# Performance work log

Measured on AMD Instinct MI355X. Metric: run time of the kernel, lower is better.

Reference implementation:

```python
import jax, jax.numpy as jnp
import numpy as np

N_NODES = 50000


def gcn_conv(x, edge_index, W, b, n_nodes):
    # Linear transform first (as in PyG GCNConv), then normalized aggregation
    xw = x @ W  # [N, out]
    src, dst = edge_index[0], edge_index[1]
    loops = jnp.arange(n_nodes, dtype=src.dtype)
    s = jnp.concatenate([src, loops])  # add self-loops
    d = jnp.concatenate([dst, loops])
    deg = jax.ops.segment_sum(jnp.ones_like(s, dtype=xw.dtype), d, num_segments=n_nodes)
    dinv = jnp.where(deg > 0, jax.lax.rsqrt(deg), 0.0)
    norm = dinv[s] * dinv[d]  # [E+N]
    msg = xw[s] * norm[:, None]  # gather + scale
    out = jax.ops.segment_sum(msg, d, num_segments=n_nodes)  # scatter-add
    return out + b


def setup_inputs() -> dict:
    key = jax.random.key(0)
    k1, k2, k3, k4 = jax.random.split(key, 4)
    in_dim, hidden = 128, 128
    n_edges = 625000
    x = jax.random.normal(k1, (N_NODES, in_dim), dtype=jnp.float32)
    edge_index = jax.random.randint(k2, (2, n_edges), 0, N_NODES, dtype=jnp.int64)
    # glorot-ish scale
    W1 = jax.random.normal(k3, (in_dim, hidden), dtype=jnp.float32) * (1.0 / np.sqrt(in_dim))
    b1 = jnp.zeros((hidden,), dtype=jnp.float32)
    W2 = jax.random.normal(k4, (hidden, hidden), dtype=jnp.float32) * (1.0 / np.sqrt(hidden))
    b2 = jnp.zeros((hidden,), dtype=jnp.float32)
    return {"x": x, "edge_index": edge_index, "W1": W1, "b1": b1, "W2": W2, "b2": b2}


def reference(x, edge_index, W1, b1, W2, b2):
    n = x.shape[0]
    h = gcn_conv(x, edge_index, W1, b1, n)
    h = jax.nn.relu(h)
    # dropout(p=0.3) is identity in eval mode
    h = gcn_conv(h, edge_index, W2, b2, n)
    return jax.nn.relu(h)
```

## Files before the change

kernel.cpp:

```cpp
#include <hip/hip_runtime.h>
#include <hip/hip_bf16.h>

#define NNODES 50000
#define BKT 64
#define LP 136

typedef short bf16x8 __attribute__((ext_vector_type(8)));
typedef float f32x4 __attribute__((ext_vector_type(4)));

__device__ __forceinline__ unsigned short f2bf_rn(float f) {
    unsigned int u = __float_as_uint(f);
    return (unsigned short)((u + 0x7fffu + ((u >> 16) & 1u)) >> 16);
}
__device__ __forceinline__ float bf_lo(unsigned int u) { return __uint_as_float(u << 16); }
__device__ __forceinline__ float bf_hi(unsigned int u) { return __uint_as_float(u & 0xffff0000u); }


__global__ __launch_bounds__(256) void k_wt(const float* __restrict__ W1,
                                            const float* __restrict__ W2,
                                            unsigned short* __restrict__ WT1,
                                            unsigned short* __restrict__ WT2,
                                            int* __restrict__ cnt, int N) {
    __shared__ float tile[128 * 129];
    int b = blockIdx.x, t = threadIdx.x;
    if (b < 2) {
        const float* W = b ? W2 : W1;
        unsigned short* WT = b ? WT2 : WT1;
        for (int idx = t; idx < 128 * 128; idx += 256)
            tile[(idx >> 7) * 129 + (idx & 127)] = W[idx];
        __syncthreads();
        for (int idx = t; idx < 128 * 128; idx += 256) {
            int c = idx >> 7, k = idx & 127;
            WT[c * 128 + k] = f2bf_rn(tile[k * 129 + c]);
        }
    } else {
        int i = (b - 2) * 256 + t;
        if (i < N) cnt[i] = 0;
    }
}


__device__ __forceinline__ void gather_accum(const unsigned int* __restrict__ xwb,
                                             const int* __restrict__ cnt,
                                             const int* __restrict__ bp,
                                             int degc, int lane,
                                             float& ax, float& ay) {
    float px = 0.f, py = 0.f;
    int j = 0;
    for (; j + 8 <= degc; j += 8) {
        int4 q0 = *(const int4*)&bp[j];
        int4 q1 = *(const int4*)&bp[j + 4];
        unsigned int u0 = xwb[(size_t)q0.x * 64 + lane];
        unsigned int u1 = xwb[(size_t)q0.y * 64 + lane];
        unsigned int u2 = xwb[(size_t)q0.z * 64 + lane];
        unsigned int u3 = xwb[(size_t)q0.w * 64 + lane];
        unsigned int u4 = xwb[(size_t)q1.x * 64 + lane];
        unsigned int u5 = xwb[(size_t)q1.y * 64 + lane];
        unsigned int u6 = xwb[(size_t)q1.z * 64 + lane];
        unsigned int u7 = xwb[(size_t)q1.w * 64 + lane];
        float w0 = rsqrtf((float)cnt[q0.x] + 1.0f), w1 = rsqrtf((float)cnt[q0.y] + 1.0f);
        float w2 = rsqrtf((float)cnt[q0.z] + 1.0f), w3 = rsqrtf((float)cnt[q0.w] + 1.0f);
        float w4 = rsqrtf((float)cnt[q1.x] + 1.0f), w5 = rsqrtf((float)cnt[q1.y] + 1.0f);
        float w6 = rsqrtf((float)cnt[q1.z] + 1.0f), w7 = rsqrtf((float)cnt[q1.w] + 1.0f);
        ax = fmaf(bf_lo(u0), w0, ax);  ay = fmaf(bf_hi(u0), w0, ay);
        px = fmaf(bf_lo(u1), w1, px);  py = fmaf(bf_hi(u1), w1, py);
        ax = fmaf(bf_lo(u2), w2, ax);  ay = fmaf(bf_hi(u2), w2, ay);
        px = fmaf(bf_lo(u3), w3, px);  py = fmaf(bf_hi(u3), w3, py);
        ax = fmaf(bf_lo(u4), w4, ax);  ay = fmaf(bf_hi(u4), w4, ay);
        px = fmaf(bf_lo(u5), w5, px);  py = fmaf(bf_hi(u5), w5, py);
        ax = fmaf(bf_lo(u6), w6, ax);  ay = fmaf(bf_hi(u6), w6, ay);
        px = fmaf(bf_lo(u7), w7, px);  py = fmaf(bf_hi(u7), w7, py);
    }
    if (j + 4 <= degc) {
        int4 q = *(const int4*)&bp[j];
        unsigned int u0 = xwb[(size_t)q.x * 64 + lane];
        unsigned int u1 = xwb[(size_t)q.y * 64 + lane];
        unsigned int u2 = xwb[(size_t)q.z * 64 + lane];
        unsigned int u3 = xwb[(size_t)q.w * 64 + lane];
        float w0 = rsqrtf((float)cnt[q.x] + 1.0f), w1 = rsqrtf((float)cnt[q.y] + 1.0f);
        float w2 = rsqrtf((float)cnt[q.z] + 1.0f), w3 = rsqrtf((float)cnt[q.w] + 1.0f);
        ax = fmaf(bf_lo(u0), w0, ax);  ay = fmaf(bf_hi(u0), w0, ay);
        px = fmaf(bf_lo(u1), w1, px);  py = fmaf(bf_hi(u1), w1, py);
        ax = fmaf(bf_lo(u2), w2, ax);  ay = fmaf(bf_hi(u2), w2, ay);
        px = fmaf(bf_lo(u3), w3, px);  py = fmaf(bf_hi(u3), w3, py);
        j += 4;
    }
    for (; j < degc; ++j) {
        int s = bp[j];
        float wv = rsqrtf((float)cnt[s] + 1.0f);
        unsigned int u = xwb[(size_t)s * 64 + lane];
        ax = fmaf(bf_lo(u), wv, ax);
        ay = fmaf(bf_hi(u), wv, ay);
    }
    ax += px;
    ay += py;
}


__global__ __launch_bounds__(256) void k_gemmbucket(const float* __restrict__ X,
                                                    const unsigned short* __restrict__ WT,
                                                    unsigned short* __restrict__ Yb, int n,
                                                    const int* __restrict__ src,
                                                    const int* __restrict__ dst,
                                                    int* __restrict__ cnt,
                                                    int* __restrict__ bkt, int E, int EB) {
    __shared__ unsigned short Wl[128 * LP];
    int t = threadIdx.x;
    if ((int)blockIdx.x < EB) {
        int e = blockIdx.x * 256 + t;
        if (e < E) {
            int s = src[e], d = dst[e];
            int pos = atomicAdd(&cnt[d], 1);
            if (pos < BKT) bkt[(size_t)d * BKT + pos] = s;
        }
        return;
    }
    int gb = blockIdx.x - EB;
    int lane = t & 63, w = t >> 6;
    int m = lane & 15, quad = lane >> 4;
    int base = gb * 64 + w * 16;
    int row = min(base + m, n - 1);

    bf16x8 a[4];
#pragma unroll
    for (int kt = 0; kt < 4; ++kt) {
        const float* pa = &X[(size_t)row * 128 + kt * 32 + quad * 8];
        float4 v0 = *(const float4*)pa;
        float4 v1 = *(const float4*)(pa + 4);
        a[kt][0] = (short)f2bf_rn(v0.x); a[kt][1] = (short)f2bf_rn(v0.y);
        a[kt][2] = (short)f2bf_rn(v0.z); a[kt][3] = (short)f2bf_rn(v0.w);
        a[kt][4] = (short)f2bf_rn(v1.x); a[kt][5] = (short)f2bf_rn(v1.y);
        a[kt][6] = (short)f2bf_rn(v1.z); a[kt][7] = (short)f2bf_rn(v1.w);
    }
    for (int idx = t; idx < 128 * 16; idx += 256) {
        int r = idx >> 4, c8 = (idx & 15) << 3;
        *(uint4*)&Wl[r * LP + c8] = *(const uint4*)&WT[r * 128 + c8];
    }
    __syncthreads();

    f32x4 acc[8];
#pragma unroll
    for (int i = 0; i < 8; ++i) acc[i] = f32x4{0.f, 0.f, 0.f, 0.f};
#pragma unroll
    for (int kt = 0; kt < 4; ++kt) {
        int ko = kt * 32 + quad * 8;
#pragma unroll
        for (int ct = 0; ct < 8; ++ct) {
            bf16x8 b = *(const bf16x8*)&Wl[(ct * 16 + m) * LP + ko];
            acc[ct] = __builtin_amdgcn_mfma_f32_16x16x32_bf16(a[kt], b, acc[ct], 0, 0, 0);
        }
    }
    __syncthreads();

    unsigned short* ep = &Wl[w * 16 * LP];
#pragma unroll
    for (int ct = 0; ct < 8; ++ct)
#pragma unroll
        for (int r = 0; r < 4; ++r)
            ep[(quad * 4 + r) * LP + ct * 16 + m] = f2bf_rn(acc[ct][r]);
    __syncthreads();
    int rr = lane & 15, cc = lane >> 4;
    int orow = base + rr;
    if (orow < n) {
#pragma unroll
        for (int i2 = 0; i2 < 4; ++i2)
            ((uint4*)&Yb[(size_t)orow * 128])[cc * 4 + i2] =
                *(const uint4*)&ep[rr * LP + (cc * 4 + i2) * 8];
    }
}


__global__ __launch_bounds__(1024, 2) void k_aggemm(const unsigned int* __restrict__ xw1,
                                                    const int* __restrict__ cnt,
                                                    const int* __restrict__ bkt,
                                                    const float* __restrict__ bias,
                                                    const unsigned short* __restrict__ WT2,
                                                    unsigned short* __restrict__ xw2, int n) {
    __shared__ unsigned short Wl[128 * LP];
    __shared__ unsigned short At[16 * LP];
    int t = threadIdx.x, lane = t & 63, w = t >> 6;
    int base = blockIdx.x * 16;

    for (int idx = t; idx < 128 * 16; idx += 1024) {
        int r = idx >> 4, c8 = (idx & 15) << 3;
        *(uint4*)&Wl[r * LP + c8] = *(const uint4*)&WT2[r * 128 + c8];
    }

    int i = min(base + w, n - 1);
    int deg = cnt[i];
    int degc = min(deg, BKT);
    float di = rsqrtf((float)deg + 1.0f);
    unsigned int v0 = xw1[(size_t)i * 64 + lane];
    float ax = di * bf_lo(v0), ay = di * bf_hi(v0);
    gather_accum(xw1, cnt, &bkt[(size_t)i * BKT], degc, lane, ax, ay);
    float bx = bias[lane * 2], by = bias[lane * 2 + 1];
    ax = fmaxf(fmaf(di, ax, bx), 0.0f);
    ay = fmaxf(fmaf(di, ay, by), 0.0f);
    ((unsigned int*)&At[w * LP])[lane] = (unsigned)f2bf_rn(ax) | ((unsigned)f2bf_rn(ay) << 16);
    __syncthreads();

    int m = lane & 15, quad = lane >> 4;
    f32x4 acc = f32x4{0.f, 0.f, 0.f, 0.f};
    if (w < 8) {
        bf16x8 a[4];
#pragma unroll
        for (int kt = 0; kt < 4; ++kt)
            a[kt] = *(const bf16x8*)&At[m * LP + kt * 32 + quad * 8];
#pragma unroll
        for (int kt = 0; kt < 4; ++kt) {
            bf16x8 b = *(const bf16x8*)&Wl[(w * 16 + m) * LP + kt * 32 + quad * 8];
            acc = __builtin_amdgcn_mfma_f32_16x16x32_bf16(a[kt], b, acc, 0, 0, 0);
        }
    }
    __syncthreads();
    if (w < 8) {
#pragma unroll
        for (int r = 0; r < 4; ++r)
            At[(quad * 4 + r) * LP + w * 16 + m] = f2bf_rn(acc[r]);
    }
    __syncthreads();
    if (t < 256) {
        int row = t >> 4, q = t & 15;
        int orow = base + row;
        if (orow < n)
            *(uint4*)&xw2[(size_t)orow * 128 + q * 8] = *(const uint4*)&At[row * LP + q * 8];
    }
}


__global__ __launch_bounds__(256) void k_agg(const unsigned int* __restrict__ xwb,
                                             const int* __restrict__ cnt,
                                             const int* __restrict__ bkt,
                                             const float* __restrict__ bias,
                                             float* __restrict__ out, int n) {
    int lane = threadIdx.x & 63;
    int i = (blockIdx.x * 256 + threadIdx.x) >> 6;
    if (i >= n) return;
    int deg = cnt[i];
    int degc = min(deg, BKT);
    float di = rsqrtf((float)deg + 1.0f);
    unsigned int v0 = xwb[(size_t)i * 64 + lane];
    float ax = di * bf_lo(v0), ay = di * bf_hi(v0);
    gather_accum(xwb, cnt, &bkt[(size_t)i * BKT], degc, lane, ax, ay);
    float bx = bias[lane * 2], by = bias[lane * 2 + 1];
    ax = fmaxf(fmaf(di, ax, bx), 0.0f);
    ay = fmaxf(fmaf(di, ay, by), 0.0f);
    ((float2*)out)[(size_t)i * 64 + lane] = make_float2(ax, ay);
}


extern "C" void kernel_launch(void* const* d_in, const int* in_sizes, int n_in,
                              void* d_out, int out_size, void* d_ws, size_t ws_size,
                              hipStream_t stream) {
    const float* x  = (const float*)d_in[0];
    const int*   ei = (const int*)d_in[1];
    const float* W1 = (const float*)d_in[2];
    const float* b1 = (const float*)d_in[3];
    const float* W2 = (const float*)d_in[4];
    const float* b2 = (const float*)d_in[5];
    float* out = (float*)d_out;

    const int N = NNODES;
    const int E = in_sizes[1] / 2;
    const int* src = ei;
    const int* dst = ei + E;

    char* p = (char*)d_ws;
    size_t off = 0;
    auto take = [&](size_t bytes) -> void* {
        void* r = p + off;
        off = (off + bytes + 255) & ~(size_t)255;
        return r;
    };
    int* cnt = (int*)take((size_t)N * 4);
    int* bkt = (int*)take((size_t)N * BKT * 4);
    unsigned short* w1t = (unsigned short*)take(128 * 128 * 2);
    unsigned short* w2t = (unsigned short*)take(128 * 128 * 2);
    unsigned short* xw1 = (unsigned short*)take((size_t)N * 128 * 2);
    unsigned short* xw2 = (unsigned short*)take((size_t)N * 128 * 2);

    const int NB = (N + 255) / 256;
    const int EB = (E + 255) / 256;
    const int GB = (N + 63) / 64;

    k_wt<<<2 + NB, 256, 0, stream>>>(W1, W2, w1t, w2t, cnt, N);
    k_gemmbucket<<<EB + GB, 256, 0, stream>>>(x, w1t, xw1, N, src, dst, cnt, bkt, E, EB);
    k_aggemm<<<(N + 15) / 16, 1024, 0, stream>>>((const unsigned int*)xw1, cnt, bkt,
                                                 b1, w2t, xw2, N);
    k_agg<<<(N * 64 + 255) / 256, 256, 0, stream>>>((const unsigned int*)xw2, cnt, bkt,
                                                    b2, out, N);
}
```

Before: 205.7 us.

## Prescale GEMM outputs by source degree norm and shrink bucket indices to u16

Folds the per-source rsqrt(deg) factor into the GEMM epilogues, so the gather loops become plain adds with no per-neighbour count lookups. Bucket indices are stored as 16-bit values, which halves index traffic. The bucketing moves into a prep kernel that handles four edges per thread, and the count reset becomes a memset. The cost is that the layer-1 GEMM now waits for bucketing to finish instead of running alongside it, and the 16-bit indices only work while the node count stays below 65536.

```diff
diff --git a/kernel.cpp b/kernel.cpp
--- a/kernel.cpp
+++ b/kernel.cpp
@@ -16,110 +16,107 @@
 __device__ __forceinline__ float bf_hi(unsigned int u) { return __uint_as_float(u & 0xffff0000u); }
 
 
-__global__ __launch_bounds__(256) void k_wt(const float* __restrict__ W1,
-                                            const float* __restrict__ W2,
-                                            unsigned short* __restrict__ WT1,
-                                            unsigned short* __restrict__ WT2,
-                                            int* __restrict__ cnt, int N) {
-    __shared__ float tile[128 * 129];
+__global__ __launch_bounds__(256) void k_prep(const float* __restrict__ W1,
+                                              const float* __restrict__ W2,
+                                              unsigned short* __restrict__ WT1,
+                                              unsigned short* __restrict__ WT2,
+                                              const int* __restrict__ src,
+                                              const int* __restrict__ dst,
+                                              int* __restrict__ cnt,
+                                              unsigned short* __restrict__ bkt,
+                                              int E, int S) {
     int b = blockIdx.x, t = threadIdx.x;
     if (b < 2) {
         const float* W = b ? W2 : W1;
         unsigned short* WT = b ? WT2 : WT1;
-        for (int idx = t; idx < 128 * 128; idx += 256)
-            tile[(idx >> 7) * 129 + (idx & 127)] = W[idx];
-        __syncthreads();
         for (int idx = t; idx < 128 * 128; idx += 256) {
-            int c = idx >> 7, k = idx & 127;
-            WT[c * 128 + k] = f2bf_rn(tile[k * 129 + c]);
+            int k = idx >> 7, c = idx & 127;
+            WT[c * 128 + k] = f2bf_rn(W[idx]);
         }
-    } else {
-        int i = (b - 2) * 256 + t;
-        if (i < N) cnt[i] = 0;
-    }
-}
-
-
-__device__ __forceinline__ void gather_accum(const unsigned int* __restrict__ xwb,
-                                             const int* __restrict__ cnt,
-                                             const int* __restrict__ bp,
-                                             int degc, int lane,
-                                             float& ax, float& ay) {
+        return;
+    }
+    int tid = (b - 2) * 256 + t;
+    int e0 = tid, e1 = tid + S, e2 = tid + 2 * S, e3 = tid + 3 * S;
+    int s0 = 0, s1 = 0, s2 = 0, s3 = 0, d0 = 0, d1 = 0, d2 = 0, d3 = 0;
+    if (e0 < E) { s0 = src[e0]; d0 = dst[e0]; }
+    if (e1 < E) { s1 = src[e1]; d1 = dst[e1]; }
+    if (e2 < E) { s2 = src[e2]; d2 = dst[e2]; }
+    if (e3 < E) { s3 = src[e3]; d3 = dst[e3]; }
+    if (e0 < E) { int p = atomicAdd(&cnt[d0], 1); if (p < BKT) bkt[(size_t)d0 * BKT + p] = (unsigned short)s0; }
+    if (e1 < E) { int p = atomicAdd(&cnt[d1], 1); if (p < BKT) bkt[(size_t)d1 * BKT + p] = (unsigned short)s1; }
+    if (e2 < E) { int p = atomicAdd(&cnt[d2], 1); if (p < BKT) bkt[(size_t)d2 * BKT + p] = (unsigned short)s2; }
+    if (e3 < E) { int p = atomicAdd(&cnt[d3], 1); if (p < BKT) bkt[(size_t)d3 * BKT + p] = (unsigned short)s3; }
+}
+
+
+__device__ __forceinline__ void gather_add(const unsigned int* __restrict__ xwb,
+                                           const unsigned short* __restrict__ bp,
+                                           int degc, int lane,
+                                           float& ax, float& ay) {
     float px = 0.f, py = 0.f;
     int j = 0;
     for (; j + 8 <= degc; j += 8) {
-        int4 q0 = *(const int4*)&bp[j];
-        int4 q1 = *(const int4*)&bp[j + 4];
-        unsigned int u0 = xwb[(size_t)q0.x * 64 + lane];
-        unsigned int u1 = xwb[(size_t)q0.y * 64 + lane];
-        unsigned int u2 = xwb[(size_t)q0.z * 64 + lane];
-        unsigned int u3 = xwb[(size_t)q0.w * 64 + lane];
-        unsigned int u4 = xwb[(size_t)q1.x * 64 + lane];
-        unsigned int u5 = xwb[(size_t)q1.y * 64 + lane];
-        unsigned int u6 = xwb[(size_t)q1.z * 64 + lane];
-        unsigned int u7 = xwb[(size_t)q1.w * 64 + lane];
-        float w0 = rsqrtf((float)cnt[q0.x] + 1.0f), w1 = rsqrtf((float)cnt[q0.y] + 1.0f);
-        float w2 = rsqrtf((float)cnt[q0.z] + 1.0f), w3 = rsqrtf((float)cnt[q0.w] + 1.0f);
-        float w4 = rsqrtf((float)cnt[q1.x] + 1.0f), w5 = rsqrtf((float)cnt[q1.y] + 1.0f);
-        float w6 = rsqrtf((float)cnt[q1.z] + 1.0f), w7 = rsqrtf((float)cnt[q1.w] + 1.0f);
-        ax = fmaf(bf_lo(u0), w0, ax);  ay = fmaf(bf_hi(u0), w0, ay);
-        px = fmaf(bf_lo(u1), w1, px);  py = fmaf(bf_hi(u1), w1, py);
-        ax = fmaf(bf_lo(u2), w2, ax);  ay = fmaf(bf_hi(u2), w2, ay);
-        px = fmaf(bf_lo(u3), w3, px);  py = fmaf(bf_hi(u3), w3, py);
-        ax = fmaf(bf_lo(u4), w4, ax);  ay = fmaf(bf_hi(u4), w4, ay);
-        px = fmaf(bf_lo(u5), w5, px);  py = fmaf(bf_hi(u5), w5, py);
-        ax = fmaf(bf_lo(u6), w6, ax);  ay = fmaf(bf_hi(u6), w6, ay);
-        px = fmaf(bf_lo(u7), w7, px);  py = fmaf(bf_hi(u7), w7, py);
+        uint4 q = *(const uint4*)&bp[j];
+        int s0 = q.x & 0xffff, s1 = q.x >> 16;
+        int s2 = q.y & 0xffff, s3 = q.y >> 16;
+        int s4 = q.z & 0xffff, s5 = q.z >> 16;
+        int s6 = q.w & 0xffff, s7 = q.w >> 16;
+        unsigned int u0 = xwb[(size_t)s0 * 64 + lane];
+        unsigned int u1 = xwb[(size_t)s1 * 64 + lane];
+        unsigned int u2 = xwb[(size_t)s2 * 64 + lane];
+        unsigned int u3 = xwb[(size_t)s3 * 64 + lane];
+        unsigned int u4 = xwb[(size_t)s4 * 64 + lane];
+        unsigned int u5 = xwb[(size_t)s5 * 64 + lane];
+        unsigned int u6 = xwb[(size_t)s6 * 64 + lane];
+        unsigned int u7 = xwb[(size_t)s7 * 64 + lane];
+        ax += bf_lo(u0);  ay += bf_hi(u0);
+        px += bf_lo(u1);  py += bf_hi(u1);
+        ax += bf_lo(u2);  ay += bf_hi(u2);
+        px += bf_lo(u3);  py += bf_hi(u3);
+        ax += bf_lo(u4);  ay += bf_hi(u4);
+        px += bf_lo(u5);  py += bf_hi(u5);
+        ax += bf_lo(u6);  ay += bf_hi(u6);
+        px += bf_lo(u7);  py += bf_hi(u7);
     }
     if (j + 4 <= degc) {
-        int4 q = *(const int4*)&bp[j];
-        unsigned int u0 = xwb[(size_t)q.x * 64 + lane];
-        unsigned int u1 = xwb[(size_t)q.y * 64 + lane];
-        unsigned int u2 = xwb[(size_t)q.z * 64 + lane];
-        unsigned int u3 = xwb[(size_t)q.w * 64 + lane];
-        float w0 = rsqrtf((float)cnt[q.x] + 1.0f), w1 = rsqrtf((float)cnt[q.y] + 1.0f);
-        float w2 = rsqrtf((float)cnt[q.z] + 1.0f), w3 = rsqrtf((float)cnt[q.w] + 1.0f);
-        ax = fmaf(bf_lo(u0), w0, ax);  ay = fmaf(bf_hi(u0), w0, ay);
-        px = fmaf(bf_lo(u1), w1, px);  py = fmaf(bf_hi(u1), w1, py);
-        ax = fmaf(bf_lo(u2), w2, ax);  ay = fmaf(bf_hi(u2), w2, ay);
-        px = fmaf(bf_lo(u3), w3, px);  py = fmaf(bf_hi(u3), w3, py);
+        uint2 q = *(const uint2*)&bp[j];
+        int s0 = q.x & 0xffff, s1 = q.x >> 16;
+        int s2 = q.y & 0xffff, s3 = q.y >> 16;
+        unsigned int u0 = xwb[(size_t)s0 * 64 + lane];
+        unsigned int u1 = xwb[(size_t)s1 * 64 + lane];
+        unsigned int u2 = xwb[(size_t)s2 * 64 + lane];
+        unsigned int u3 = xwb[(size_t)s3 * 64 + lane];
+        ax += bf_lo(u0);  ay += bf_hi(u0);
+        px += bf_lo(u1);  py += bf_hi(u1);
+        ax += bf_lo(u2);  ay += bf_hi(u2);
+        px += bf_lo(u3);  py += bf_hi(u3);
         j += 4;
     }
     for (; j < degc; ++j) {
         int s = bp[j];
-        float wv = rsqrtf((float)cnt[s] + 1.0f);
         unsigned int u = xwb[(size_t)s * 64 + lane];
-        ax = fmaf(bf_lo(u), wv, ax);
-        ay = fmaf(bf_hi(u), wv, ay);
+        ax += bf_lo(u);
+        ay += bf_hi(u);
     }
     ax += px;
     ay += py;
 }
 
 
-__global__ __launch_bounds__(256) void k_gemmbucket(const float* __restrict__ X,
-                                                    const unsigned short* __restrict__ WT,
-                                                    unsigned short* __restrict__ Yb, int n,
-                                                    const int* __restrict__ src,
-                                                    const int* __restrict__ dst,
-                                                    int* __restrict__ cnt,
-                                                    int* __restrict__ bkt, int E, int EB) {
+__global__ __launch_bounds__(256) void k_gemm1(const float* __restrict__ X,
+                                               const unsigned short* __restrict__ WT,
+                                               const int* __restrict__ cnt,
+                                               unsigned short* __restrict__ Yb, int n) {
     __shared__ unsigned short Wl[128 * LP];
-    int t = threadIdx.x;
-    if ((int)blockIdx.x < EB) {
-        int e = blockIdx.x * 256 + t;
-        if (e < E) {
-            int s = src[e], d = dst[e];
-            int pos = atomicAdd(&cnt[d], 1);
-            if (pos < BKT) bkt[(size_t)d * BKT + pos] = s;
-        }
-        return;
-    }
-    int gb = blockIdx.x - EB;
-    int lane = t & 63, w = t >> 6;
+    int t = threadIdx.x, lane = t & 63, w = t >> 6;
     int m = lane & 15, quad = lane >> 4;
-    int base = gb * 64 + w * 16;
+    int base = blockIdx.x * 64 + w * 16;
     int row = min(base + m, n - 1);
+
+    float di_r[4];
+#pragma unroll
+    for (int r = 0; r < 4; ++r)
+        di_r[r] = rsqrtf((float)cnt[min(base + quad * 4 + r, n - 1)] + 1.0f);
 
     bf16x8 a[4];
 #pragma unroll
@@ -146,8 +143,8 @@
         int ko = kt * 32 + quad * 8;
 #pragma unroll
         for (int ct = 0; ct < 8; ++ct) {
-            bf16x8 b = *(const bf16x8*)&Wl[(ct * 16 + m) * LP + ko];
-            acc[ct] = __builtin_amdgcn_mfma_f32_16x16x32_bf16(a[kt], b, acc[ct], 0, 0, 0);
+            bf16x8 bb = *(const bf16x8*)&Wl[(ct * 16 + m) * LP + ko];
+            acc[ct] = __builtin_amdgcn_mfma_f32_16x16x32_bf16(a[kt], bb, acc[ct], 0, 0, 0);
         }
     }
     __syncthreads();
@@ -157,7 +154,7 @@
     for (int ct = 0; ct < 8; ++ct)
 #pragma unroll
         for (int r = 0; r < 4; ++r)
-            ep[(quad * 4 + r) * LP + ct * 16 + m] = f2bf_rn(acc[ct][r]);
+            ep[(quad * 4 + r) * LP + ct * 16 + m] = f2bf_rn(acc[ct][r] * di_r[r]);
     __syncthreads();
     int rr = lane & 15, cc = lane >> 4;
     int orow = base + rr;
@@ -172,14 +169,20 @@
 
 __global__ __launch_bounds__(1024, 2) void k_aggemm(const unsigned int* __restrict__ xw1,
                                                     const int* __restrict__ cnt,
-                                                    const int* __restrict__ bkt,
+                                                    const unsigned short* __restrict__ bkt,
                                                     const float* __restrict__ bias,
                                                     const unsigned short* __restrict__ WT2,
                                                     unsigned short* __restrict__ xw2, int n) {
     __shared__ unsigned short Wl[128 * LP];
     __shared__ unsigned short At[16 * LP];
     int t = threadIdx.x, lane = t & 63, w = t >> 6;
+    int m = lane & 15, quad = lane >> 4;
     int base = blockIdx.x * 16;
+
+    float di_e[4];
+#pragma unroll
+    for (int r = 0; r < 4; ++r)
+        di_e[r] = rsqrtf((float)cnt[min(base + quad * 4 + r, n - 1)] + 1.0f);
 
     for (int idx = t; idx < 128 * 16; idx += 1024) {
         int r = idx >> 4, c8 = (idx & 15) << 3;
@@ -191,15 +194,14 @@
     int degc = min(deg, BKT);
     float di = rsqrtf((float)deg + 1.0f);
     unsigned int v0 = xw1[(size_t)i * 64 + lane];
-    float ax = di * bf_lo(v0), ay = di * bf_hi(v0);
-    gather_accum(xw1, cnt, &bkt[(size_t)i * BKT], degc, lane, ax, ay);
+    float ax = bf_lo(v0), ay = bf_hi(v0);
+    gather_add(xw1, &bkt[(size_t)i * BKT], degc, lane, ax, ay);
     float bx = bias[lane * 2], by = bias[lane * 2 + 1];
     ax = fmaxf(fmaf(di, ax, bx), 0.0f);
     ay = fmaxf(fmaf(di, ay, by), 0.0f);
     ((unsigned int*)&At[w * LP])[lane] = (unsigned)f2bf_rn(ax) | ((unsigned)f2bf_rn(ay) << 16);
     __syncthreads();
 
-    int m = lane & 15, quad = lane >> 4;
     f32x4 acc = f32x4{0.f, 0.f, 0.f, 0.f};
     if (w < 8) {
         bf16x8 a[4];
@@ -208,15 +210,15 @@
             a[kt] = *(const bf16x8*)&At[m * LP + kt * 32 + quad * 8];
 #pragma unroll
         for (int kt = 0; kt < 4; ++kt) {
-            bf16x8 b = *(const bf16x8*)&Wl[(w * 16 + m) * LP + kt * 32 + quad * 8];
-            acc = __builtin_amdgcn_mfma_f32_16x16x32_bf16(a[kt], b, acc, 0, 0, 0);
+            bf16x8 bb = *(const bf16x8*)&Wl[(w * 16 + m) * LP + kt * 32 + quad * 8];
+            acc = __builtin_amdgcn_mfma_f32_16x16x32_bf16(a[kt], bb, acc, 0, 0, 0);
         }
     }
     __syncthreads();
     if (w < 8) {
 #pragma unroll
         for (int r = 0; r < 4; ++r)
-            At[(quad * 4 + r) * LP + w * 16 + m] = f2bf_rn(acc[r]);
+            At[(quad * 4 + r) * LP + w * 16 + m] = f2bf_rn(acc[r] * di_e[r]);
     }
     __syncthreads();
     if (t < 256) {
@@ -230,7 +232,7 @@
 
 __global__ __launch_bounds__(256) void k_agg(const unsigned int* __restrict__ xwb,
                                              const int* __restrict__ cnt,
-                                             const int* __restrict__ bkt,
+                                             const unsigned short* __restrict__ bkt,
                                              const float* __restrict__ bias,
                                              float* __restrict__ out, int n) {
     int lane = threadIdx.x & 63;
@@ -240,8 +242,8 @@
     int degc = min(deg, BKT);
     float di = rsqrtf((float)deg + 1.0f);
     unsigned int v0 = xwb[(size_t)i * 64 + lane];
-    float ax = di * bf_lo(v0), ay = di * bf_hi(v0);
-    gather_accum(xwb, cnt, &bkt[(size_t)i * BKT], degc, lane, ax, ay);
+    float ax = bf_lo(v0), ay = bf_hi(v0);
+    gather_add(xwb, &bkt[(size_t)i * BKT], degc, lane, ax, ay);
     float bx = bias[lane * 2], by = bias[lane * 2 + 1];
     ax = fmaxf(fmaf(di, ax, bx), 0.0f);
     ay = fmaxf(fmaf(di, ay, by), 0.0f);
@@ -273,18 +275,19 @@
         return r;
     };
     int* cnt = (int*)take((size_t)N * 4);
-    int* bkt = (int*)take((size_t)N * BKT * 4);
+    unsigned short* bkt = (unsigned short*)take((size_t)N * BKT * 2);
     unsigned short* w1t = (unsigned short*)take(128 * 128 * 2);
     unsigned short* w2t = (unsigned short*)take(128 * 128 * 2);
     unsigned short* xw1 = (unsigned short*)take((size_t)N * 128 * 2);
     unsigned short* xw2 = (unsigned short*)take((size_t)N * 128 * 2);
 
-    const int NB = (N + 255) / 256;
-    const int EB = (E + 255) / 256;
+    const int BB = (E + 4 * 256 - 1) / (4 * 256);
+    const int S  = BB * 256;
     const int GB = (N + 63) / 64;
 
-    k_wt<<<2 + NB, 256, 0, stream>>>(W1, W2, w1t, w2t, cnt, N);
-    k_gemmbucket<<<EB + GB, 256, 0, stream>>>(x, w1t, xw1, N, src, dst, cnt, bkt, E, EB);
+    hipMemsetAsync(cnt, 0, (size_t)N * 4, stream);
+    k_prep<<<2 + BB, 256, 0, stream>>>(W1, W2, w1t, w2t, src, dst, cnt, bkt, E, S);
+    k_gemm1<<<GB, 256, 0, stream>>>(x, w1t, cnt, xw1, N);
     k_aggemm<<<(N + 15) / 16, 1024, 0, stream>>>((const unsigned int*)xw1, cnt, bkt,
                                                  b1, w2t, xw2, N);
     k_agg<<<(N * 64 + 255) / 256, 256, 0, stream>>>((const unsigned int*)xw2, cnt, bkt,
```

New measurement: 211.9 us. 3.0% more time.

## Pack neighbor indices to 16-bit, gather with 16-byte loads, prescale second-layer features

Applied to the files above, without the earlier changes.

Bucket indices are stored as unsigned short instead of int, which halves bucket memory traffic. The aggregation kernels now map four nodes per wavefront, with 16 lanes each loading 16-byte vectors instead of 4-byte words. The layer-2 GEMM output is pre-multiplied by the source node's dinv, so the final aggregation skips the per-neighbor count lookups and rsqrt. The fused aggregation-GEMM kernel also processes 64 rows per block instead of 16. Risks: 16-bit indices only hold node ids below 65536, and loop predication now runs by wavefront via __any.

```diff
diff --git a/kernel.cpp b/kernel.cpp
--- a/kernel.cpp
+++ b/kernel.cpp
@@ -14,6 +14,13 @@
 }
 __device__ __forceinline__ float bf_lo(unsigned int u) { return __uint_as_float(u << 16); }
 __device__ __forceinline__ float bf_hi(unsigned int u) { return __uint_as_float(u & 0xffff0000u); }
+
+__device__ __forceinline__ void acc8(float* a, uint4 u, float wv) {
+    a[0] = fmaf(bf_lo(u.x), wv, a[0]);  a[1] = fmaf(bf_hi(u.x), wv, a[1]);
+    a[2] = fmaf(bf_lo(u.y), wv, a[2]);  a[3] = fmaf(bf_hi(u.y), wv, a[3]);
+    a[4] = fmaf(bf_lo(u.z), wv, a[4]);  a[5] = fmaf(bf_hi(u.z), wv, a[5]);
+    a[6] = fmaf(bf_lo(u.w), wv, a[6]);  a[7] = fmaf(bf_hi(u.w), wv, a[7]);
+}
 
 
 __global__ __launch_bounds__(256) void k_wt(const float* __restrict__ W1,
@@ -40,70 +47,14 @@
 }
 
 
-__device__ __forceinline__ void gather_accum(const unsigned int* __restrict__ xwb,
-                                             const int* __restrict__ cnt,
-                                             const int* __restrict__ bp,
-                                             int degc, int lane,
-                                             float& ax, float& ay) {
-    float px = 0.f, py = 0.f;
-    int j = 0;
-    for (; j + 8 <= degc; j += 8) {
-        int4 q0 = *(const int4*)&bp[j];
-        int4 q1 = *(const int4*)&bp[j + 4];
-        unsigned int u0 = xwb[(size_t)q0.x * 64 + lane];
-        unsigned int u1 = xwb[(size_t)q0.y * 64 + lane];
-        unsigned int u2 = xwb[(size_t)q0.z * 64 + lane];
-        unsigned int u3 = xwb[(size_t)q0.w * 64 + lane];
-        unsigned int u4 = xwb[(size_t)q1.x * 64 + lane];
-        unsigned int u5 = xwb[(size_t)q1.y * 64 + lane];
-        unsigned int u6 = xwb[(size_t)q1.z * 64 + lane];
-        unsigned int u7 = xwb[(size_t)q1.w * 64 + lane];
-        float w0 = rsqrtf((float)cnt[q0.x] + 1.0f), w1 = rsqrtf((float)cnt[q0.y] + 1.0f);
-        float w2 = rsqrtf((float)cnt[q0.z] + 1.0f), w3 = rsqrtf((float)cnt[q0.w] + 1.0f);
-        float w4 = rsqrtf((float)cnt[q1.x] + 1.0f), w5 = rsqrtf((float)cnt[q1.y] + 1.0f);
-        float w6 = rsqrtf((float)cnt[q1.z] + 1.0f), w7 = rsqrtf((float)cnt[q1.w] + 1.0f);
-        ax = fmaf(bf_lo(u0), w0, ax);  ay = fmaf(bf_hi(u0), w0, ay);
-        px = fmaf(bf_lo(u1), w1, px);  py = fmaf(bf_hi(u1), w1, py);
-        ax = fmaf(bf_lo(u2), w2, ax);  ay = fmaf(bf_hi(u2), w2, ay);
-        px = fmaf(bf_lo(u3), w3, px);  py = fmaf(bf_hi(u3), w3, py);
-        ax = fmaf(bf_lo(u4), w4, ax);  ay = fmaf(bf_hi(u4), w4, ay);
-        px = fmaf(bf_lo(u5), w5, px);  py = fmaf(bf_hi(u5), w5, py);
-        ax = fmaf(bf_lo(u6), w6, ax);  ay = fmaf(bf_hi(u6), w6, ay);
-        px = fmaf(bf_lo(u7), w7, px);  py = fmaf(bf_hi(u7), w7, py);
-    }
-    if (j + 4 <= degc) {
-        int4 q = *(const int4*)&bp[j];
-        unsigned int u0 = xwb[(size_t)q.x * 64 + lane];
-        unsigned int u1 = xwb[(size_t)q.y * 64 + lane];
-        unsigned int u2 = xwb[(size_t)q.z * 64 + lane];
-        unsigned int u3 = xwb[(size_t)q.w * 64 + lane];
-        float w0 = rsqrtf((float)cnt[q.x] + 1.0f), w1 = rsqrtf((float)cnt[q.y] + 1.0f);
-        float w2 = rsqrtf((float)cnt[q.z] + 1.0f), w3 = rsqrtf((float)cnt[q.w] + 1.0f);
-        ax = fmaf(bf_lo(u0), w0, ax);  ay = fmaf(bf_hi(u0), w0, ay);
-        px = fmaf(bf_lo(u1), w1, px);  py = fmaf(bf_hi(u1), w1, py);
-        ax = fmaf(bf_lo(u2), w2, ax);  ay = fmaf(bf_hi(u2), w2, ay);
-        px = fmaf(bf_lo(u3), w3, px);  py = fmaf(bf_hi(u3), w3, py);
-        j += 4;
-    }
-    for (; j < degc; ++j) {
-        int s = bp[j];
-        float wv = rsqrtf((float)cnt[s] + 1.0f);
-        unsigned int u = xwb[(size_t)s * 64 + lane];
-        ax = fmaf(bf_lo(u), wv, ax);
-        ay = fmaf(bf_hi(u), wv, ay);
-    }
-    ax += px;
-    ay += py;
-}
-
-
 __global__ __launch_bounds__(256) void k_gemmbucket(const float* __restrict__ X,
                                                     const unsigned short* __restrict__ WT,
                                                     unsigned short* __restrict__ Yb, int n,
                                                     const int* __restrict__ src,
                                                     const int* __restrict__ dst,
                                                     int* __restrict__ cnt,
-                                                    int* __restrict__ bkt, int E, int EB) {
+                                                    unsigned short* __restrict__ bkt,
+                                                    int E, int EB) {
     __shared__ unsigned short Wl[128 * LP];
     int t = threadIdx.x;
     if ((int)blockIdx.x < EB) {
@@ -111,7 +62,7 @@
         if (e < E) {
             int s = src[e], d = dst[e];
             int pos = atomicAdd(&cnt[d], 1);
-            if (pos < BKT) bkt[(size_t)d * BKT + pos] = s;
+            if (pos < BKT) bkt[(size_t)d * BKT + pos] = (unsigned short)s;
         }
         return;
     }
@@ -146,8 +97,8 @@
         int ko = kt * 32 + quad * 8;
 #pragma unroll
         for (int ct = 0; ct < 8; ++ct) {
-            bf16x8 b = *(const bf16x8*)&Wl[(ct * 16 + m) * LP + ko];
-            acc[ct] = __builtin_amdgcn_mfma_f32_16x16x32_bf16(a[kt], b, acc[ct], 0, 0, 0);
+            bf16x8 bb = *(const bf16x8*)&Wl[(ct * 16 + m) * LP + ko];
+            acc[ct] = __builtin_amdgcn_mfma_f32_16x16x32_bf16(a[kt], bb, acc[ct], 0, 0, 0);
         }
     }
     __syncthreads();
@@ -170,82 +121,159 @@
 }
 
 
-__global__ __launch_bounds__(1024, 2) void k_aggemm(const unsigned int* __restrict__ xw1,
+__global__ __launch_bounds__(1024, 2) void k_aggemm(const unsigned int* __restrict__ xw1u,
                                                     const int* __restrict__ cnt,
-                                                    const int* __restrict__ bkt,
+                                                    const unsigned short* __restrict__ bkt,
                                                     const float* __restrict__ bias,
                                                     const unsigned short* __restrict__ WT2,
                                                     unsigned short* __restrict__ xw2, int n) {
     __shared__ unsigned short Wl[128 * LP];
-    __shared__ unsigned short At[16 * LP];
+    __shared__ unsigned short At[64 * LP];
     int t = threadIdx.x, lane = t & 63, w = t >> 6;
-    int base = blockIdx.x * 16;
+    int base = blockIdx.x * 64;
 
     for (int idx = t; idx < 128 * 16; idx += 1024) {
         int r = idx >> 4, c8 = (idx & 15) << 3;
         *(uint4*)&Wl[r * LP + c8] = *(const uint4*)&WT2[r * 128 + c8];
     }
 
-    int i = min(base + w, n - 1);
-    int deg = cnt[i];
-    int degc = min(deg, BKT);
+    int g = lane >> 4, li = lane & 15;
+    int node = min(base + w * 4 + g, n - 1);
+    int deg = cnt[node], degc = min(deg, BKT);
     float di = rsqrtf((float)deg + 1.0f);
-    unsigned int v0 = xw1[(size_t)i * 64 + lane];
-    float ax = di * bf_lo(v0), ay = di * bf_hi(v0);
-    gather_accum(xw1, cnt, &bkt[(size_t)i * BKT], degc, lane, ax, ay);
-    float bx = bias[lane * 2], by = bias[lane * 2 + 1];
-    ax = fmaxf(fmaf(di, ax, bx), 0.0f);
-    ay = fmaxf(fmaf(di, ay, by), 0.0f);
-    ((unsigned int*)&At[w * LP])[lane] = (unsigned)f2bf_rn(ax) | ((unsigned)f2bf_rn(ay) << 16);
-    __syncthreads();
+    uint4 v = *(const uint4*)&xw1u[(size_t)node * 64 + li * 4];
+    float a[8];
+    a[0] = di * bf_lo(v.x);  a[1] = di * bf_hi(v.x);
+    a[2] = di * bf_lo(v.y);  a[3] = di * bf_hi(v.y);
+    a[4] = di * bf_lo(v.z);  a[5] = di * bf_hi(v.z);
+    a[6] = di * bf_lo(v.w);  a[7] = di * bf_hi(v.w);
+    const unsigned short* bp = &bkt[(size_t)node * BKT];
+    for (int j = 0; __any(j < degc); j += 8) {
+        if (j < degc) {
+            uint4 q = *(const uint4*)&bp[j];
+            int s0 = q.x & 0xffff, s1 = q.x >> 16, s2 = q.y & 0xffff, s3 = q.y >> 16;
+            int s4 = q.z & 0xffff, s5 = q.z >> 16, s6 = q.w & 0xffff, s7 = q.w >> 16;
+            uint4 u0 = *(const uint4*)&xw1u[(size_t)s0 * 64 + li * 4];
+            uint4 u1 = *(const uint4*)&xw1u[(size_t)s1 * 64 + li * 4];
+            uint4 u2 = *(const uint4*)&xw1u[(size_t)s2 * 64 + li * 4];
+            uint4 u3 = *(const uint4*)&xw1u[(size_t)s3 * 64 + li * 4];
+            uint4 u4 = *(const uint4*)&xw1u[(size_t)s4 * 64 + li * 4];
+            uint4 u5 = *(const uint4*)&xw1u[(size_t)s5 * 64 + li * 4];
+            uint4 u6 = *(const uint4*)&xw1u[(size_t)s6 * 64 + li * 4];
+            uint4 u7 = *(const uint4*)&xw1u[(size_t)s7 * 64 + li * 4];
+            float w0 = (j + 0 < degc) ? rsqrtf((float)cnt[s0] + 1.0f) : 0.0f;
+            float w1 = (j + 1 < degc) ? rsqrtf((float)cnt[s1] + 1.0f) : 0.0f;
+            float w2 = (j + 2 < degc) ? rsqrtf((float)cnt[s2] + 1.0f) : 0.0f;
+            float w3 = (j + 3 < degc) ? rsqrtf((float)cnt[s3] + 1.0f) : 0.0f;
+            float w4 = (j + 4 < degc) ? rsqrtf((float)cnt[s4] + 1.0f) : 0.0f;
+            float w5 = (j + 5 < degc) ? rsqrtf((float)cnt[s5] + 1.0f) : 0.0f;
+            float w6 = (j + 6 < degc) ? rsqrtf((float)cnt[s6] + 1.0f) : 0.0f;
+            float w7 = (j + 7 < degc) ? rsqrtf((float)cnt[s7] + 1.0f) : 0.0f;
+            acc8(a, u0, w0); acc8(a, u1, w1); acc8(a, u2, w2); acc8(a, u3, w3);
+            acc8(a, u4, w4); acc8(a, u5, w5); acc8(a, u6, w6); acc8(a, u7, w7);
+        }
+    }
+    float4 b0 = ((const float4*)bias)[li * 2];
+    float4 b1v = ((const float4*)bias)[li * 2 + 1];
+    float h0 = fmaxf(fmaf(di, a[0], b0.x), 0.f), h1 = fmaxf(fmaf(di, a[1], b0.y), 0.f);
+    float h2 = fmaxf(fmaf(di, a[2], b0.z), 0.f), h3 = fmaxf(fmaf(di, a[3], b0.w), 0.f);
+    float h4 = fmaxf(fmaf(di, a[4], b1v.x), 0.f), h5 = fmaxf(fmaf(di, a[5], b1v.y), 0.f);
+    float h6 = fmaxf(fmaf(di, a[6], b1v.z), 0.f), h7 = fmaxf(fmaf(di, a[7], b1v.w), 0.f);
+    uint4 hp;
+    hp.x = (unsigned)f2bf_rn(h0) | ((unsigned)f2bf_rn(h1) << 16);
+    hp.y = (unsigned)f2bf_rn(h2) | ((unsigned)f2bf_rn(h3) << 16);
+    hp.z = (unsigned)f2bf_rn(h4) | ((unsigned)f2bf_rn(h5) << 16);
+    hp.w = (unsigned)f2bf_rn(h6) | ((unsigned)f2bf_rn(h7) << 16);
+    *(uint4*)&At[(w * 4 + g) * LP + li * 8] = hp;
 
     int m = lane & 15, quad = lane >> 4;
-    f32x4 acc = f32x4{0.f, 0.f, 0.f, 0.f};
-    if (w < 8) {
-        bf16x8 a[4];
-#pragma unroll
-        for (int kt = 0; kt < 4; ++kt)
-            a[kt] = *(const bf16x8*)&At[m * LP + kt * 32 + quad * 8];
-#pragma unroll
-        for (int kt = 0; kt < 4; ++kt) {
-            bf16x8 b = *(const bf16x8*)&Wl[(w * 16 + m) * LP + kt * 32 + quad * 8];
-            acc = __builtin_amdgcn_mfma_f32_16x16x32_bf16(a[kt], b, acc, 0, 0, 0);
-        }
-    }
-    __syncthreads();
-    if (w < 8) {
+    int ct = w & 7, mt2 = (w >> 3) * 2;
+    float die[2][4];
+#pragma unroll
+    for (int mt = 0; mt < 2; ++mt)
 #pragma unroll
         for (int r = 0; r < 4; ++r)
-            At[(quad * 4 + r) * LP + w * 16 + m] = f2bf_rn(acc[r]);
-    }
-    __syncthreads();
-    if (t < 256) {
-        int row = t >> 4, q = t & 15;
-        int orow = base + row;
+            die[mt][r] = rsqrtf(
+                (float)cnt[min(base + (mt2 + mt) * 16 + quad * 4 + r, n - 1)] + 1.0f);
+    __syncthreads();
+
+    f32x4 acc0 = f32x4{0.f, 0.f, 0.f, 0.f};
+    f32x4 acc1 = f32x4{0.f, 0.f, 0.f, 0.f};
+#pragma unroll
+    for (int kt = 0; kt < 4; ++kt) {
+        int ko = kt * 32 + quad * 8;
+        bf16x8 bb = *(const bf16x8*)&Wl[(ct * 16 + m) * LP + ko];
+        bf16x8 aA = *(const bf16x8*)&At[(mt2 * 16 + m) * LP + ko];
+        bf16x8 aB = *(const bf16x8*)&At[((mt2 + 1) * 16 + m) * LP + ko];
+        acc0 = __builtin_amdgcn_mfma_f32_16x16x32_bf16(aA, bb, acc0, 0, 0, 0);
+        acc1 = __builtin_amdgcn_mfma_f32_16x16x32_bf16(aB, bb, acc1, 0, 0, 0);
+    }
+    __syncthreads();
+#pragma unroll
+    for (int r = 0; r < 4; ++r) {
+        At[(mt2 * 16 + quad * 4 + r) * LP + ct * 16 + m] = f2bf_rn(acc0[r] * die[0][r]);
+        At[((mt2 + 1) * 16 + quad * 4 + r) * LP + ct * 16 + m] = f2bf_rn(acc1[r] * die[1][r]);
+    }
+    __syncthreads();
+    {
+        int rowi = t >> 4, q = t & 15;
+        int orow = base + rowi;
         if (orow < n)
-            *(uint4*)&xw2[(size_t)orow * 128 + q * 8] = *(const uint4*)&At[row * LP + q * 8];
-    }
-}
-
-
-__global__ __launch_bounds__(256) void k_agg(const unsigned int* __restrict__ xwb,
+            *(uint4*)&xw2[(size_t)orow * 128 + q * 8] = *(const uint4*)&At[rowi * LP + q * 8];
+    }
+}
+
+
+__global__ __launch_bounds__(256) void k_agg(const unsigned int* __restrict__ xw2u,
                                              const int* __restrict__ cnt,
-                                             const int* __restrict__ bkt,
+                                             const unsigned short* __restrict__ bkt,
                                              const float* __restrict__ bias,
                                              float* __restrict__ out, int n) {
-    int lane = threadIdx.x & 63;
-    int i = (blockIdx.x * 256 + threadIdx.x) >> 6;
-    if (i >= n) return;
-    int deg = cnt[i];
-    int degc = min(deg, BKT);
+    int t = threadIdx.x, lane = t & 63, w = t >> 6;
+    int g = lane >> 4, li = lane & 15;
+    int node = blockIdx.x * 16 + w * 4 + g;
+    int nc = min(node, n - 1);
+    int deg = cnt[nc], degc = min(deg, BKT);
     float di = rsqrtf((float)deg + 1.0f);
-    unsigned int v0 = xwb[(size_t)i * 64 + lane];
-    float ax = di * bf_lo(v0), ay = di * bf_hi(v0);
-    gather_accum(xwb, cnt, &bkt[(size_t)i * BKT], degc, lane, ax, ay);
-    float bx = bias[lane * 2], by = bias[lane * 2 + 1];
-    ax = fmaxf(fmaf(di, ax, bx), 0.0f);
-    ay = fmaxf(fmaf(di, ay, by), 0.0f);
-    ((float2*)out)[(size_t)i * 64 + lane] = make_float2(ax, ay);
+    uint4 v = *(const uint4*)&xw2u[(size_t)nc * 64 + li * 4];
+    float a[8];
+    a[0] = bf_lo(v.x);  a[1] = bf_hi(v.x);
+    a[2] = bf_lo(v.y);  a[3] = bf_hi(v.y);
+    a[4] = bf_lo(v.z);  a[5] = bf_hi(v.z);
+    a[6] = bf_lo(v.w);  a[7] = bf_hi(v.w);
+    const unsigned short* bp = &bkt[(size_t)nc * BKT];
+    for (int j = 0; __any(j < degc); j += 8) {
+        if (j < degc) {
+            uint4 q = *(const uint4*)&bp[j];
+            int s0 = q.x & 0xffff, s1 = q.x >> 16, s2 = q.y & 0xffff, s3 = q.y >> 16;
+            int s4 = q.z & 0xffff, s5 = q.z >> 16, s6 = q.w & 0xffff, s7 = q.w >> 16;
+            uint4 u0 = *(const uint4*)&xw2u[(size_t)s0 * 64 + li * 4];
+            uint4 u1 = *(const uint4*)&xw2u[(size_t)s1 * 64 + li * 4];
+            uint4 u2 = *(const uint4*)&xw2u[(size_t)s2 * 64 + li * 4];
+            uint4 u3 = *(const uint4*)&xw2u[(size_t)s3 * 64 + li * 4];
+            uint4 u4 = *(const uint4*)&xw2u[(size_t)s4 * 64 + li * 4];
+            uint4 u5 = *(const uint4*)&xw2u[(size_t)s5 * 64 + li * 4];
+            uint4 u6 = *(const uint4*)&xw2u[(size_t)s6 * 64 + li * 4];
+            uint4 u7 = *(const uint4*)&xw2u[(size_t)s7 * 64 + li * 4];
+            float w0 = (j + 0 < degc) ? 1.0f : 0.0f, w1 = (j + 1 < degc) ? 1.0f : 0.0f;
+            float w2 = (j + 2 < degc) ? 1.0f : 0.0f, w3 = (j + 3 < degc) ? 1.0f : 0.0f;
+            float w4 = (j + 4 < degc) ? 1.0f : 0.0f, w5 = (j + 5 < degc) ? 1.0f : 0.0f;
+            float w6 = (j + 6 < degc) ? 1.0f : 0.0f, w7 = (j + 7 < degc) ? 1.0f : 0.0f;
+            acc8(a, u0, w0); acc8(a, u1, w1); acc8(a, u2, w2); acc8(a, u3, w3);
+            acc8(a, u4, w4); acc8(a, u5, w5); acc8(a, u6, w6); acc8(a, u7, w7);
+        }
+    }
+    float4 b0 = ((const float4*)bias)[li * 2];
+    float4 b1v = ((const float4*)bias)[li * 2 + 1];
+    float4 o0, o1;
+    o0.x = fmaxf(fmaf(di, a[0], b0.x), 0.f);  o0.y = fmaxf(fmaf(di, a[1], b0.y), 0.f);
+    o0.z = fmaxf(fmaf(di, a[2], b0.z), 0.f);  o0.w = fmaxf(fmaf(di, a[3], b0.w), 0.f);
+    o1.x = fmaxf(fmaf(di, a[4], b1v.x), 0.f); o1.y = fmaxf(fmaf(di, a[5], b1v.y), 0.f);
+    o1.z = fmaxf(fmaf(di, a[6], b1v.z), 0.f); o1.w = fmaxf(fmaf(di, a[7], b1v.w), 0.f);
+    if (node < n) {
+        *(float4*)&out[(size_t)node * 128 + li * 8] = o0;
+        *(float4*)&out[(size_t)node * 128 + li * 8 + 4] = o1;
+    }
 }
 
 
@@ -273,7 +301,7 @@
         return r;
     };
     int* cnt = (int*)take((size_t)N * 4);
-    int* bkt = (int*)take((size_t)N * BKT * 4);
+    unsigned short* bkt = (unsigned short*)take((size_t)N * BKT * 2);
     unsigned short* w1t = (unsigned short*)take(128 * 128 * 2);
     unsigned short* w2t = (unsigned short*)take(128 * 128 * 2);
     unsigned short* xw1 = (unsigned short*)take((size_t)N * 128 * 2);
@@ -282,11 +310,10 @@
     const int NB = (N + 255) / 256;
     const int EB = (E + 255) / 256;
     const int GB = (N + 63) / 64;
+    const int AB = (N + 15) / 16;
 
     k_wt<<<2 + NB, 256, 0, stream>>>(W1, W2, w1t, w2t, cnt, N);
     k_gemmbucket<<<EB + GB, 256, 0, stream>>>(x, w1t, xw1, N, src, dst, cnt, bkt, E, EB);
-    k_aggemm<<<(N + 15) / 16, 1024, 0, stream>>>((const unsigned int*)xw1, cnt, bkt,
-                                                 b1, w2t, xw2, N);
-    k_agg<<<(N * 64 + 255) / 256, 256, 0, stream>>>((const unsigned int*)xw2, cnt, bkt,
-                                                    b2, out, N);
-}
+    k_aggemm<<<GB, 1024, 0, stream>>>((const unsigned int*)xw1, cnt, bkt, b1, w2t, xw2, N);
+    k_agg<<<AB, 256, 0, stream>>>((const unsigned int*)xw2, cnt, bkt, b2, out, N);
+}
```

After: 209.5 us. About the same (+1.9%).
